# Kernel tuning notes

Hardware: AMD Instinct MI355X
Metric: run time of the kernel (lower is better)

Reference implementation:

```python
import jax, jax.numpy as jnp
import numpy as np

N_NODES = 100000
N_EDGES = 400000
IN_DIM = 69        # torchdrug default atom feature dim
HIDDEN = 256
NUM_CLASSES = 2
NUM_GRAPHS = 4096


def gcn_conv(x, W, b, src, dst, n_nodes):
    """PyG GCNConv: out = D^{-1/2}(A+I)D^{-1/2} (x W) + b (self-loops added)."""
    h = x @ W  # [N, out_dim]
    loop = jnp.arange(n_nodes, dtype=src.dtype)
    s = jnp.concatenate([src, loop])  # sources incl. self loops
    d = jnp.concatenate([dst, loop])  # targets incl. self loops
    deg = jax.ops.segment_sum(jnp.ones_like(d, dtype=h.dtype), d, num_segments=n_nodes)
    dinv = jnp.where(deg > 0, jax.lax.rsqrt(deg), 0.0)
    norm = dinv[s] * dinv[d]  # [E+N]
    msgs = h[s] * norm[:, None]  # gather + scale
    out = jax.ops.segment_sum(msgs, d, num_segments=n_nodes)  # scatter-add
    return out + b


def setup_inputs() -> dict:
    key = jax.random.key(0)
    ks = jax.random.split(key, 16)
    x = jax.random.normal(ks[0], (N_NODES, IN_DIM), dtype=jnp.float32)
    edge_index = jax.random.randint(ks[1], (2, N_EDGES), 0, N_NODES, dtype=jnp.int64)
    batch = jnp.sort(jax.random.randint(ks[2], (N_NODES,), 0, NUM_GRAPHS, dtype=jnp.int64))

    def glorot(k, fan_in, fan_out):
        lim = np.sqrt(6.0 / (fan_in + fan_out)).astype(np.float32)
        return jax.random.uniform(k, (fan_in, fan_out), jnp.float32, -lim, lim)

    W1 = glorot(ks[3], IN_DIM, HIDDEN)
    W2 = glorot(ks[4], HIDDEN, HIDDEN)
    W3 = glorot(ks[5], HIDDEN, HIDDEN)
    W4 = glorot(ks[6], HIDDEN, HIDDEN)
    b1 = jnp.zeros((HIDDEN,), jnp.float32)
    b2 = jnp.zeros((HIDDEN,), jnp.float32)
    b3 = jnp.zeros((HIDDEN,), jnp.float32)
    b4 = jnp.zeros((HIDDEN,), jnp.float32)
    Wl = glorot(ks[7], HIDDEN, NUM_CLASSES)
    bl = jnp.zeros((NUM_CLASSES,), jnp.float32)
    return {"x": x, "edge_index": edge_index, "batch": batch,
            "W1": W1, "b1": b1, "W2": W2, "b2": b2,
            "W3": W3, "b3": b3, "W4": W4, "b4": b4,
            "Wl": Wl, "bl": bl}


def reference(x, edge_index, batch, W1, b1, W2, b2, W3, b3, W4, b4, Wl, bl):
    src, dst = edge_index[0], edge_index[1]
    n = x.shape[0]
    h = jax.nn.relu(gcn_conv(x, W1, b1, src, dst, n))
    h = jax.nn.relu(gcn_conv(h, W2, b2, src, dst, n))
    h = jax.nn.relu(gcn_conv(h, W3, b3, src, dst, n))
    h = gcn_conv(h, W4, b4, src, dst, n)
    # global_mean_pool
    sums = jax.ops.segment_sum(h, batch, num_segments=NUM_GRAPHS)  # [G, H]
    cnts = jax.ops.segment_sum(jnp.ones((n,), h.dtype), batch, num_segments=NUM_GRAPHS)
    pooled = sums / jnp.maximum(cnts, 1.0)[:, None]
    # dropout is identity in eval mode
    return pooled @ Wl + bl  # [G, num_classes]
```

## Files before the change

kernel.cpp:

```cpp
#include <hip/hip_runtime.h>
#include <hip/hip_bf16.h>

#define N_NODES 100000
#define N_EDGES 400000
#define IN_DIM  69
#define KP1     96
#define HID     256
#define NG      4096
#define SCAN_B  391

typedef __attribute__((ext_vector_type(8))) short bf16x8;
typedef __attribute__((ext_vector_type(4))) float f32x4;
typedef unsigned short u16;
typedef unsigned int   u32;

__device__ __forceinline__ float b2f(u16 v) {
    u32 x = ((u32)v) << 16;
    return __builtin_bit_cast(float, x);
}
__device__ __forceinline__ u16 f2b(float f) {
    u32 x = __builtin_bit_cast(u32, f);
    u32 r = (x + 0x7FFF + ((x >> 16) & 1)) >> 16;
    return (u16)r;
}
__device__ __forceinline__ float lo16(u32 v) { return b2f((u16)(v & 0xffff)); }
__device__ __forceinline__ float hi16(u32 v) { return b2f((u16)(v >> 16)); }

__global__ void k_deg(const int* __restrict__ dst, int* __restrict__ deg) {
    int e = blockIdx.x * blockDim.x + threadIdx.x;
    if (e < N_EDGES) atomicAdd(&deg[dst[e]], 1);
}

__global__ void k_dinv(const int* __restrict__ deg, float* __restrict__ dinv) {
    int n = blockIdx.x * blockDim.x + threadIdx.x;
    if (n < N_NODES) dinv[n] = rsqrtf((float)deg[n] + 1.0f);
}

__global__ void k_scan_local(const int* __restrict__ deg, int* __restrict__ rowptr,
                             int* __restrict__ bsum) {
    __shared__ int s[256];
    int tid = threadIdx.x;
    int i = blockIdx.x * 256 + tid;
    int v = (i < N_NODES) ? deg[i] : 0;
    s[tid] = v;
    __syncthreads();
    #pragma unroll
    for (int off = 1; off < 256; off <<= 1) {
        int t = 0;
        if (tid >= off) t = s[tid - off];
        __syncthreads();
        if (tid >= off) s[tid] += t;
        __syncthreads();
    }
    if (i < N_NODES) rowptr[i] = s[tid] - v;
    if (tid == 255) bsum[blockIdx.x] = s[255];
}

__global__ void k_scan_bsum(int* __restrict__ bsum, int* __restrict__ boff) {
    __shared__ int s[512];
    int tid = threadIdx.x;
    int v = (tid < SCAN_B) ? bsum[tid] : 0;
    s[tid] = v;
    __syncthreads();
    #pragma unroll
    for (int off = 1; off < 512; off <<= 1) {
        int t = 0;
        if (tid >= off) t = s[tid - off];
        __syncthreads();
        if (tid >= off) s[tid] += t;
        __syncthreads();
    }
    if (tid < SCAN_B) boff[tid] = s[tid] - v;
}

__global__ void k_scan_add(int* __restrict__ rowptr, const int* __restrict__ boff) {
    int i = blockIdx.x * 256 + threadIdx.x;
    if (i < N_NODES) rowptr[i] += boff[blockIdx.x];
    if (i == 0) rowptr[N_NODES] = N_EDGES;
}

__global__ void k_fill(const int* __restrict__ src, const int* __restrict__ dst,
                       const int* __restrict__ rowptr, int* __restrict__ fill,
                       int* __restrict__ col) {
    int e = blockIdx.x * blockDim.x + threadIdx.x;
    if (e < N_EDGES) {
        int d = dst[e];
        int pos = rowptr[d] + atomicAdd(&fill[d], 1);
        col[pos] = src[e];
    }
}

__global__ void k_gptr(const int* __restrict__ batch, int* __restrict__ gptr) {
    int g = blockIdx.x * 256 + threadIdx.x;
    if (g > NG) return;
    if (g == NG) { gptr[NG] = N_NODES; return; }
    int lo = 0, hi = N_NODES;
    while (lo < hi) {
        int mid = (lo + hi) >> 1;
        if (batch[mid] < g) lo = mid + 1; else hi = mid;
    }
    gptr[g] = lo;
}

__global__ void k_transpose_w(const float* __restrict__ W, u16* __restrict__ Wt, int K, int KP) {
    int k = blockIdx.x;
    int n = threadIdx.x;
    Wt[(size_t)n * KP + k] = (k < K) ? f2b(W[(size_t)k * HID + n]) : (u16)0;
}

__global__ __launch_bounds__(256) void k_pad_scale(const float* __restrict__ x,
                                                   const float* __restrict__ dinv,
                                                   u16* __restrict__ xs) {
    int node = blockIdx.x * 4 + (threadIdx.x >> 6);
    if (node >= N_NODES) return;
    int lane = threadIdx.x & 63;
    if (lane >= 48) return;
    int d0 = lane * 2, d1 = lane * 2 + 1;
    float dv = dinv[node];
    const float* xr = x + (size_t)node * IN_DIM;
    float v0 = (d0 < IN_DIM) ? xr[d0] * dv : 0.0f;
    float v1 = (d1 < IN_DIM) ? xr[d1] * dv : 0.0f;
    u32 o = (u32)f2b(v0) | ((u32)f2b(v1) << 16);
    *(u32*)(xs + (size_t)node * KP1 + d0) = o;
}

__global__ __launch_bounds__(256) void k_agg96(const int* __restrict__ rowptr,
                                               const int* __restrict__ col,
                                               const u16* __restrict__ xs,
                                               const float* __restrict__ dinv,
                                               u16* __restrict__ xa) {
    int node = blockIdx.x * 4 + (threadIdx.x >> 6);
    if (node >= N_NODES) return;
    int lane = threadIdx.x & 63;
    if (lane >= 48) return;
    int j = lane * 2;

    u32 v = *(const u32*)(xs + (size_t)node * KP1 + j);
    float a0 = lo16(v), a1 = hi16(v);
    int e = rowptr[node], end = rowptr[node + 1];
    for (; e + 4 <= end; e += 4) {
        int s0 = col[e], s1 = col[e + 1], s2 = col[e + 2], s3 = col[e + 3];
        u32 w0 = *(const u32*)(xs + (size_t)s0 * KP1 + j);
        u32 w1 = *(const u32*)(xs + (size_t)s1 * KP1 + j);
        u32 w2 = *(const u32*)(xs + (size_t)s2 * KP1 + j);
        u32 w3 = *(const u32*)(xs + (size_t)s3 * KP1 + j);
        a0 += (lo16(w0) + lo16(w1)) + (lo16(w2) + lo16(w3));
        a1 += (hi16(w0) + hi16(w1)) + (hi16(w2) + hi16(w3));
    }
    for (; e < end; ++e) {
        u32 w = *(const u32*)(xs + (size_t)col[e] * KP1 + j);
        a0 += lo16(w); a1 += hi16(w);
    }
    float dv = dinv[node];
    u32 o = (u32)f2b(a0 * dv) | ((u32)f2b(a1 * dv) << 16);
    *(u32*)(xa + (size_t)node * KP1 + j) = o;
}

template<int MODE>
__global__ __launch_bounds__(256) void k_gemm(const u16* __restrict__ A, int KP, int M,
                                              const u16* __restrict__ Wt,
                                              const float* __restrict__ dinv,
                                              const float* __restrict__ bias,
                                              u16* __restrict__ Out) {
    __shared__ __align__(16) u16 As[64 * 40];
    __shared__ __align__(16) u16 Bs[256 * 40];

    const int tid  = threadIdx.x;
    const int wave = tid >> 6;
    const int lane = tid & 63;
    const int quad = lane >> 4;
    const int lm   = lane & 15;
    const int m0   = blockIdx.x * 64;

    f32x4 acc[4][4] = {};

    const int ar = tid >> 2;
    const int ai = (tid & 3) * 8;

    for (int kt = 0; kt < KP; kt += 32) {
        __syncthreads();
        {
            int m = m0 + ar;
            uint4 v = make_uint4(0, 0, 0, 0);
            if (m < M) v = *(const uint4*)(A + (size_t)m * KP + kt + ai);
            *(uint4*)(As + ar * 40 + ai) = v;
        }
        #pragma unroll
        for (int p = 0; p < 4; ++p) {
            int n = p * 64 + (tid >> 2);
            uint4 v = *(const uint4*)(Wt + (size_t)n * KP + kt + ai);
            *(uint4*)(Bs + n * 40 + ai) = v;
        }
        __syncthreads();

        bf16x8 af[4], bfr[4];
        #pragma unroll
        for (int rt = 0; rt < 4; ++rt)
            af[rt] = *(const bf16x8*)(As + (rt * 16 + lm) * 40 + quad * 8);
        #pragma unroll
        for (int ct = 0; ct < 4; ++ct)
            bfr[ct] = *(const bf16x8*)(Bs + (wave * 64 + ct * 16 + lm) * 40 + quad * 8);
        #pragma unroll
        for (int rt = 0; rt < 4; ++rt)
            #pragma unroll
            for (int ct = 0; ct < 4; ++ct)
                acc[rt][ct] = __builtin_amdgcn_mfma_f32_16x16x32_bf16(af[rt], bfr[ct], acc[rt][ct], 0, 0, 0);
    }

    #pragma unroll
    for (int rt = 0; rt < 4; ++rt) {
        #pragma unroll
        for (int reg = 0; reg < 4; ++reg) {
            int m = m0 + rt * 16 + quad * 4 + reg;
            if (m >= M) continue;
            float dv = (MODE == 0) ? dinv[m] : 0.0f;
            #pragma unroll
            for (int ct = 0; ct < 4; ++ct) {
                int n = wave * 64 + ct * 16 + lm;
                float v = acc[rt][ct][reg];
                if (MODE == 0) v *= dv;
                else           v = fmaxf(v + bias[n], 0.0f);
                Out[(size_t)m * HID + n] = f2b(v);
            }
        }
    }
}

__global__ __launch_bounds__(256) void k_agg256(const int* __restrict__ rowptr,
                                                const int* __restrict__ col,
                                                const u16* __restrict__ g,
                                                const float* __restrict__ dinv,
                                                const float* __restrict__ bias,
                                                u16* __restrict__ Xout) {
    int node = blockIdx.x * 4 + (threadIdx.x >> 6);
    if (node >= N_NODES) return;
    int lane = threadIdx.x & 63;
    int j = lane * 4;
    const u16* gj = g + j;

    float a0, a1, a2, a3;
    {
        uint2 v = *(const uint2*)(gj + (size_t)node * HID);
        a0 = lo16(v.x); a1 = hi16(v.x); a2 = lo16(v.y); a3 = hi16(v.y);
    }
    int e = rowptr[node], end = rowptr[node + 1];
    for (; e + 4 <= end; e += 4) {
        int s0 = col[e], s1 = col[e + 1], s2 = col[e + 2], s3 = col[e + 3];
        uint2 w0 = *(const uint2*)(gj + (size_t)s0 * HID);
        uint2 w1 = *(const uint2*)(gj + (size_t)s1 * HID);
        uint2 w2 = *(const uint2*)(gj + (size_t)s2 * HID);
        uint2 w3 = *(const uint2*)(gj + (size_t)s3 * HID);
        a0 += (lo16(w0.x) + lo16(w1.x)) + (lo16(w2.x) + lo16(w3.x));
        a1 += (hi16(w0.x) + hi16(w1.x)) + (hi16(w2.x) + hi16(w3.x));
        a2 += (lo16(w0.y) + lo16(w1.y)) + (lo16(w2.y) + lo16(w3.y));
        a3 += (hi16(w0.y) + hi16(w1.y)) + (hi16(w2.y) + hi16(w3.y));
    }
    for (; e < end; ++e) {
        int s = col[e];
        uint2 w = *(const uint2*)(gj + (size_t)s * HID);
        a0 += lo16(w.x); a1 += hi16(w.x); a2 += lo16(w.y); a3 += hi16(w.y);
    }
    float dv = dinv[node];
    float4 bb = *(const float4*)(bias + j);
    a0 = fmaxf(fmaf(a0, dv, bb.x), 0.0f);
    a1 = fmaxf(fmaf(a1, dv, bb.y), 0.0f);
    a2 = fmaxf(fmaf(a2, dv, bb.z), 0.0f);
    a3 = fmaxf(fmaf(a3, dv, bb.w), 0.0f);
    uint2 o;
    o.x = (u32)f2b(a0) | ((u32)f2b(a1) << 16);
    o.y = (u32)f2b(a2) | ((u32)f2b(a3) << 16);
    *(uint2*)(Xout + (size_t)node * HID + j) = o;
}

__global__ void k_w4l(const float* __restrict__ W4, const float* __restrict__ Wl,
                      const float* __restrict__ b4, const float* __restrict__ bl,
                      float* __restrict__ W4l, float* __restrict__ c4) {
    int k = threadIdx.x;
    float s0 = 0.0f, s1 = 0.0f;
    const float* wr = W4 + (size_t)k * HID;
    for (int j = 0; j < HID; ++j) {
        float w = wr[j];
        s0 += w * Wl[j * 2 + 0];
        s1 += w * Wl[j * 2 + 1];
    }
    W4l[k * 2 + 0] = s0;
    W4l[k * 2 + 1] = s1;
    if (k < 2) {
        float s = bl[k];
        for (int j = 0; j < HID; ++j) s += b4[j] * Wl[j * 2 + k];
        c4[k] = s;
    }
}

__global__ __launch_bounds__(256) void k_gemm2col(const u16* __restrict__ X,
                                                  const float* __restrict__ W4l,
                                                  const float* __restrict__ dinv,
                                                  float* __restrict__ g4) {
    __shared__ float2 sW[HID];
    int tid = threadIdx.x;
    sW[tid] = *(const float2*)(W4l + tid * 2);
    __syncthreads();

    int node = blockIdx.x * 4 + (tid >> 6);
    if (node >= N_NODES) return;
    int lane = tid & 63;
    uint2 v = *(const uint2*)(X + (size_t)node * HID + lane * 4);
    float x0 = lo16(v.x), x1 = hi16(v.x), x2 = lo16(v.y), x3 = hi16(v.y);
    float2 w0 = sW[lane * 4 + 0], w1 = sW[lane * 4 + 1];
    float2 w2 = sW[lane * 4 + 2], w3 = sW[lane * 4 + 3];
    float s0 = x0 * w0.x + x1 * w1.x + x2 * w2.x + x3 * w3.x;
    float s1 = x0 * w0.y + x1 * w1.y + x2 * w2.y + x3 * w3.y;
    #pragma unroll
    for (int off = 32; off >= 1; off >>= 1) {
        s0 += __shfl_down(s0, off);
        s1 += __shfl_down(s1, off);
    }
    if (lane == 0) {
        float dv = dinv[node];
        *(float2*)(g4 + (size_t)node * 2) = make_float2(s0 * dv, s1 * dv);
    }
}

__global__ void k_agg2(const int* __restrict__ rowptr, const int* __restrict__ col,
                       const float* __restrict__ g4, const float* __restrict__ dinv,
                       float* __restrict__ h4) {
    int node = blockIdx.x * blockDim.x + threadIdx.x;
    if (node >= N_NODES) return;
    float2 a = *(const float2*)(g4 + (size_t)node * 2);
    int e = rowptr[node], end = rowptr[node + 1];
    for (; e < end; ++e) {
        float2 w = *(const float2*)(g4 + (size_t)col[e] * 2);
        a.x += w.x; a.y += w.y;
    }
    float dv = dinv[node];
    *(float2*)(h4 + (size_t)node * 2) = make_float2(a.x * dv, a.y * dv);
}

__global__ __launch_bounds__(256) void k_pool2(const float* __restrict__ h4,
                                               const int* __restrict__ gptr,
                                               const float* __restrict__ c4,
                                               float* __restrict__ out) {
    int gph = blockIdx.x * 4 + (threadIdx.x >> 6);
    if (gph >= NG) return;
    int lane = threadIdx.x & 63;
    int b = gptr[gph], e = gptr[gph + 1];
    float s0 = 0.0f, s1 = 0.0f;
    for (int n = b + lane; n < e; n += 64) {
        float2 v = *(const float2*)(h4 + (size_t)n * 2);
        s0 += v.x; s1 += v.y;
    }
    #pragma unroll
    for (int off = 32; off >= 1; off >>= 1) {
        s0 += __shfl_down(s0, off);
        s1 += __shfl_down(s1, off);
    }
    if (lane == 0) {
        float inv = 1.0f / fmaxf((float)(e - b), 1.0f);
        out[gph * 2 + 0] = s0 * inv + c4[0];
        out[gph * 2 + 1] = s1 * inv + c4[1];
    }
}

extern "C" void kernel_launch(void* const* d_in, const int* in_sizes, int n_in,
                              void* d_out, int out_size, void* d_ws, size_t ws_size,
                              hipStream_t stream) {
    const float* x   = (const float*)d_in[0];
    const int* ei    = (const int*)d_in[1];
    const int* src   = ei;
    const int* dst   = ei + N_EDGES;
    const int* batch = (const int*)d_in[2];
    const float* W1 = (const float*)d_in[3];  const float* b1 = (const float*)d_in[4];
    const float* W2 = (const float*)d_in[5];  const float* b2 = (const float*)d_in[6];
    const float* W3 = (const float*)d_in[7];  const float* b3 = (const float*)d_in[8];
    const float* W4 = (const float*)d_in[9];  const float* b4 = (const float*)d_in[10];
    const float* Wl = (const float*)d_in[11]; const float* bl = (const float*)d_in[12];
    float* out = (float*)d_out;

    char* p = (char*)d_ws;
    auto take = [&](size_t bytes) { char* r = p; p += (bytes + 255) & ~(size_t)255; return r; };
    size_t zbytes = (size_t)(N_NODES + N_NODES) * 4;
    int*   deg  = (int*)take(zbytes);
    int*   fill = deg + N_NODES;
    float* dinv = (float*)take((size_t)N_NODES * sizeof(float));
    int* rowptr = (int*)take((size_t)(N_NODES + 1) * sizeof(int));
    int* col    = (int*)take((size_t)N_EDGES * sizeof(int));
    int* bsum   = (int*)take((size_t)SCAN_B * sizeof(int));
    int* boff   = (int*)take((size_t)SCAN_B * sizeof(int));
    int* gptr   = (int*)take((size_t)(NG + 1) * sizeof(int));
    float* W4l  = (float*)take((size_t)HID * 2 * sizeof(float));
    float* c4   = (float*)take(2 * sizeof(float));
    float* g4   = (float*)take((size_t)N_NODES * 2 * sizeof(float));
    float* h4   = (float*)take((size_t)N_NODES * 2 * sizeof(float));
    u16* Wt1 = (u16*)take((size_t)HID * KP1 * 2);
    u16* Wt2 = (u16*)take((size_t)HID * HID * 2);
    u16* Wt3 = (u16*)take((size_t)HID * HID * 2);
    u16* Xs  = (u16*)take((size_t)N_NODES * KP1 * 2);
    u16* Xa  = (u16*)take((size_t)N_NODES * KP1 * 2);
    u16* Gbuf = (u16*)take((size_t)N_NODES * HID * 2);
    u16* Xbuf = (u16*)take((size_t)N_NODES * HID * 2);

    hipMemsetAsync(deg, 0, zbytes, stream);

    k_deg<<<(N_EDGES + 255) / 256, 256, 0, stream>>>(dst, deg);
    k_scan_local<<<SCAN_B, 256, 0, stream>>>(deg, rowptr, bsum);
    k_scan_bsum<<<1, 512, 0, stream>>>(bsum, boff);
    k_scan_add<<<SCAN_B, 256, 0, stream>>>(rowptr, boff);
    k_fill<<<(N_EDGES + 255) / 256, 256, 0, stream>>>(src, dst, rowptr, fill, col);
    k_dinv<<<(N_NODES + 255) / 256, 256, 0, stream>>>(deg, dinv);
    k_gptr<<<(NG + 256) / 256, 256, 0, stream>>>(batch, gptr);

    k_transpose_w<<<KP1, 256, 0, stream>>>(W1, Wt1, IN_DIM, KP1);
    k_transpose_w<<<HID, 256, 0, stream>>>(W2, Wt2, HID, HID);
    k_transpose_w<<<HID, 256, 0, stream>>>(W3, Wt3, HID, HID);
    k_w4l<<<1, 256, 0, stream>>>(W4, Wl, b4, bl, W4l, c4);

    const int gemm_grid = (N_NODES + 63) / 64;
    const int nb4       = (N_NODES + 3) / 4;

    k_pad_scale<<<nb4, 256, 0, stream>>>(x, dinv, Xs);
    k_agg96<<<nb4, 256, 0, stream>>>(rowptr, col, Xs, dinv, Xa);
    k_gemm<1><<<gemm_grid, 256, 0, stream>>>(Xa, KP1, N_NODES, Wt1, dinv, b1, Xbuf);
    k_gemm<0><<<gemm_grid, 256, 0, stream>>>(Xbuf, HID, N_NODES, Wt2, dinv, b2, Gbuf);
    k_agg256<<<nb4, 256, 0, stream>>>(rowptr, col, Gbuf, dinv, b2, Xbuf);
    k_gemm<0><<<gemm_grid, 256, 0, stream>>>(Xbuf, HID, N_NODES, Wt3, dinv, b3, Gbuf);
    k_agg256<<<nb4, 256, 0, stream>>>(rowptr, col, Gbuf, dinv, b3, Xbuf);
    k_gemm2col<<<nb4, 256, 0, stream>>>(Xbuf, W4l, dinv, g4);
    k_agg2<<<(N_NODES + 255) / 256, 256, 0, stream>>>(rowptr, col, g4, dinv, h4);
    k_pool2<<<(NG + 3) / 4, 256, 0, stream>>>(h4, gptr, c4, out);
}
```

Before: 440.1 us.

## Retile GEMM to 128x128 with direct global-to-LDS loads and merge prep kernels

The GEMM moves from 64-row tiles covering all 256 columns to 128x128 tiles on a 2D grid, with a K step of 64. Tiles are loaded with global_load_lds into XOR-swizzled shared memory, which avoids a register round trip and bank conflicts. Row bounds checks are dropped by padding the activation buffers to a multiple of 128 rows, and the first layer's K is padded to 128. The dinv computation is folded into the scan, and the weight transposes, W4·Wl fold and graph-pointer search are merged into one launch to cut launch overhead. The risks are reading uninitialised padded rows, which only produce discarded outputs, and the extra work from padding K for layer 1.

```diff
diff --git a/kernel.cpp b/kernel.cpp
--- a/kernel.cpp
+++ b/kernel.cpp
@@ -2,9 +2,11 @@
 #include <hip/hip_bf16.h>
 
 #define N_NODES 100000
+#define M_PAD   100096
 #define N_EDGES 400000
 #define IN_DIM  69
-#define KP1     96
+#define KPX     96
+#define KPA     128
 #define HID     256
 #define NG      4096
 #define SCAN_B  391
@@ -26,22 +28,24 @@
 __device__ __forceinline__ float lo16(u32 v) { return b2f((u16)(v & 0xffff)); }
 __device__ __forceinline__ float hi16(u32 v) { return b2f((u16)(v >> 16)); }
 
+__device__ __forceinline__ void gl_lds16(const u16* g, u16* l) {
+    __builtin_amdgcn_global_load_lds(
+        (const __attribute__((address_space(1))) void*)g,
+        (__attribute__((address_space(3))) void*)l, 16, 0, 0);
+}
+
 __global__ void k_deg(const int* __restrict__ dst, int* __restrict__ deg) {
     int e = blockIdx.x * blockDim.x + threadIdx.x;
     if (e < N_EDGES) atomicAdd(&deg[dst[e]], 1);
 }
 
-__global__ void k_dinv(const int* __restrict__ deg, float* __restrict__ dinv) {
-    int n = blockIdx.x * blockDim.x + threadIdx.x;
-    if (n < N_NODES) dinv[n] = rsqrtf((float)deg[n] + 1.0f);
-}
-
 __global__ void k_scan_local(const int* __restrict__ deg, int* __restrict__ rowptr,
-                             int* __restrict__ bsum) {
+                             int* __restrict__ bsum, float* __restrict__ dinv) {
     __shared__ int s[256];
     int tid = threadIdx.x;
     int i = blockIdx.x * 256 + tid;
     int v = (i < N_NODES) ? deg[i] : 0;
+    if (i < N_NODES) dinv[i] = rsqrtf((float)v + 1.0f);
     s[tid] = v;
     __syncthreads();
     #pragma unroll
@@ -90,22 +94,48 @@
     }
 }
 
-__global__ void k_gptr(const int* __restrict__ batch, int* __restrict__ gptr) {
-    int g = blockIdx.x * 256 + threadIdx.x;
-    if (g > NG) return;
-    if (g == NG) { gptr[NG] = N_NODES; return; }
-    int lo = 0, hi = N_NODES;
-    while (lo < hi) {
-        int mid = (lo + hi) >> 1;
-        if (batch[mid] < g) lo = mid + 1; else hi = mid;
-    }
-    gptr[g] = lo;
-}
-
-__global__ void k_transpose_w(const float* __restrict__ W, u16* __restrict__ Wt, int K, int KP) {
-    int k = blockIdx.x;
-    int n = threadIdx.x;
-    Wt[(size_t)n * KP + k] = (k < K) ? f2b(W[(size_t)k * HID + n]) : (u16)0;
+__global__ void k_prep(const float* __restrict__ W1, const float* __restrict__ W2,
+                       const float* __restrict__ W3, const float* __restrict__ W4,
+                       const float* __restrict__ Wl, const float* __restrict__ b4,
+                       const float* __restrict__ bl, const int* __restrict__ batch,
+                       u16* __restrict__ Wt1, u16* __restrict__ Wt2, u16* __restrict__ Wt3,
+                       float* __restrict__ W4l, float* __restrict__ c4, int* __restrict__ gptr) {
+    int b = blockIdx.x;
+    int t = threadIdx.x;
+    if (b < KPA) {
+        Wt1[(size_t)t * KPA + b] = (b < IN_DIM) ? f2b(W1[(size_t)b * HID + t]) : (u16)0;
+    } else if (b < KPA + HID) {
+        int k = b - KPA;
+        Wt2[(size_t)t * HID + k] = f2b(W2[(size_t)k * HID + t]);
+    } else if (b < KPA + 2 * HID) {
+        int k = b - KPA - HID;
+        Wt3[(size_t)t * HID + k] = f2b(W3[(size_t)k * HID + t]);
+    } else if (b == KPA + 2 * HID) {
+        float s0 = 0.0f, s1 = 0.0f;
+        const float* wr = W4 + (size_t)t * HID;
+        for (int j = 0; j < HID; ++j) {
+            float w = wr[j];
+            s0 += w * Wl[j * 2 + 0];
+            s1 += w * Wl[j * 2 + 1];
+        }
+        W4l[t * 2 + 0] = s0;
+        W4l[t * 2 + 1] = s1;
+        if (t < 2) {
+            float s = bl[t];
+            for (int j = 0; j < HID; ++j) s += b4[j] * Wl[j * 2 + t];
+            c4[t] = s;
+        }
+    } else {
+        int g = (b - (KPA + 2 * HID + 1)) * 256 + t;
+        if (g > NG) return;
+        if (g == NG) { gptr[NG] = N_NODES; return; }
+        int lo = 0, hi = N_NODES;
+        while (lo < hi) {
+            int mid = (lo + hi) >> 1;
+            if (batch[mid] < g) lo = mid + 1; else hi = mid;
+        }
+        gptr[g] = lo;
+    }
 }
 
 __global__ __launch_bounds__(256) void k_pad_scale(const float* __restrict__ x,
@@ -121,7 +151,7 @@
     float v0 = (d0 < IN_DIM) ? xr[d0] * dv : 0.0f;
     float v1 = (d1 < IN_DIM) ? xr[d1] * dv : 0.0f;
     u32 o = (u32)f2b(v0) | ((u32)f2b(v1) << 16);
-    *(u32*)(xs + (size_t)node * KP1 + d0) = o;
+    *(u32*)(xs + (size_t)node * KPX + d0) = o;
 }
 
 __global__ __launch_bounds__(256) void k_agg96(const int* __restrict__ rowptr,
@@ -132,91 +162,98 @@
     int node = blockIdx.x * 4 + (threadIdx.x >> 6);
     if (node >= N_NODES) return;
     int lane = threadIdx.x & 63;
-    if (lane >= 48) return;
+    if (lane >= 48) {
+        *(u32*)(xa + (size_t)node * KPA + lane * 2) = 0;
+        return;
+    }
     int j = lane * 2;
-
-    u32 v = *(const u32*)(xs + (size_t)node * KP1 + j);
+    u32 v = *(const u32*)(xs + (size_t)node * KPX + j);
     float a0 = lo16(v), a1 = hi16(v);
     int e = rowptr[node], end = rowptr[node + 1];
     for (; e + 4 <= end; e += 4) {
         int s0 = col[e], s1 = col[e + 1], s2 = col[e + 2], s3 = col[e + 3];
-        u32 w0 = *(const u32*)(xs + (size_t)s0 * KP1 + j);
-        u32 w1 = *(const u32*)(xs + (size_t)s1 * KP1 + j);
-        u32 w2 = *(const u32*)(xs + (size_t)s2 * KP1 + j);
-        u32 w3 = *(const u32*)(xs + (size_t)s3 * KP1 + j);
+        u32 w0 = *(const u32*)(xs + (size_t)s0 * KPX + j);
+        u32 w1 = *(const u32*)(xs + (size_t)s1 * KPX + j);
+        u32 w2 = *(const u32*)(xs + (size_t)s2 * KPX + j);
+        u32 w3 = *(const u32*)(xs + (size_t)s3 * KPX + j);
         a0 += (lo16(w0) + lo16(w1)) + (lo16(w2) + lo16(w3));
         a1 += (hi16(w0) + hi16(w1)) + (hi16(w2) + hi16(w3));
     }
     for (; e < end; ++e) {
-        u32 w = *(const u32*)(xs + (size_t)col[e] * KP1 + j);
+        u32 w = *(const u32*)(xs + (size_t)col[e] * KPX + j);
         a0 += lo16(w); a1 += hi16(w);
     }
     float dv = dinv[node];
     u32 o = (u32)f2b(a0 * dv) | ((u32)f2b(a1 * dv) << 16);
-    *(u32*)(xa + (size_t)node * KP1 + j) = o;
+    *(u32*)(xa + (size_t)node * KPA + j) = o;
 }
 
 template<int MODE>
-__global__ __launch_bounds__(256) void k_gemm(const u16* __restrict__ A, int KP, int M,
+__global__ __launch_bounds__(256) void k_gemm(const u16* __restrict__ A, int KP,
                                               const u16* __restrict__ Wt,
                                               const float* __restrict__ dinv,
                                               const float* __restrict__ bias,
                                               u16* __restrict__ Out) {
-    __shared__ __align__(16) u16 As[64 * 40];
-    __shared__ __align__(16) u16 Bs[256 * 40];
+    __shared__ __align__(16) u16 As[128 * 64];
+    __shared__ __align__(16) u16 Bs[128 * 64];
 
     const int tid  = threadIdx.x;
     const int wave = tid >> 6;
     const int lane = tid & 63;
     const int quad = lane >> 4;
     const int lm   = lane & 15;
-    const int m0   = blockIdx.x * 64;
+    const int wr   = wave >> 1;
+    const int wc   = wave & 1;
+    const int m0   = blockIdx.x * 128;
+    const int n0   = blockIdx.y * 128;
 
     f32x4 acc[4][4] = {};
 
-    const int ar = tid >> 2;
-    const int ai = (tid & 3) * 8;
-
-    for (int kt = 0; kt < KP; kt += 32) {
-        __syncthreads();
-        {
-            int m = m0 + ar;
-            uint4 v = make_uint4(0, 0, 0, 0);
-            if (m < M) v = *(const uint4*)(A + (size_t)m * KP + kt + ai);
-            *(uint4*)(As + ar * 40 + ai) = v;
-        }
+    const int sr = lane >> 3;
+    const int sc = lane & 7;
+    const int gc = sc ^ (sr & 7);
+
+    for (int kt = 0; kt < KP; kt += 64) {
+        __syncthreads();
         #pragma unroll
-        for (int p = 0; p < 4; ++p) {
-            int n = p * 64 + (tid >> 2);
-            uint4 v = *(const uint4*)(Wt + (size_t)n * KP + kt + ai);
-            *(uint4*)(Bs + n * 40 + ai) = v;
-        }
-        __syncthreads();
-
-        bf16x8 af[4], bfr[4];
+        for (int i = 0; i < 4; ++i) {
+            int s = wave * 4 + i;
+            int r = s * 8 + sr;
+            const u16* ga = A  + (size_t)(m0 + r) * KP + kt + gc * 8;
+            const u16* gb = Wt + (size_t)(n0 + r) * KP + kt + gc * 8;
+            gl_lds16(ga, As + s * 512);
+            gl_lds16(gb, Bs + s * 512);
+        }
+        __syncthreads();
+
         #pragma unroll
-        for (int rt = 0; rt < 4; ++rt)
-            af[rt] = *(const bf16x8*)(As + (rt * 16 + lm) * 40 + quad * 8);
-        #pragma unroll
-        for (int ct = 0; ct < 4; ++ct)
-            bfr[ct] = *(const bf16x8*)(Bs + (wave * 64 + ct * 16 + lm) * 40 + quad * 8);
-        #pragma unroll
-        for (int rt = 0; rt < 4; ++rt)
+        for (int st = 0; st < 2; ++st) {
+            bf16x8 af[4], bfr[4];
+            const int slot = ((st * 4 + quad) ^ (lm & 7)) * 8;
+            #pragma unroll
+            for (int rt = 0; rt < 4; ++rt)
+                af[rt] = *(const bf16x8*)(As + (wr * 64 + rt * 16 + lm) * 64 + slot);
             #pragma unroll
             for (int ct = 0; ct < 4; ++ct)
-                acc[rt][ct] = __builtin_amdgcn_mfma_f32_16x16x32_bf16(af[rt], bfr[ct], acc[rt][ct], 0, 0, 0);
+                bfr[ct] = *(const bf16x8*)(Bs + (wc * 64 + ct * 16 + lm) * 64 + slot);
+            #pragma unroll
+            for (int rt = 0; rt < 4; ++rt)
+                #pragma unroll
+                for (int ct = 0; ct < 4; ++ct)
+                    acc[rt][ct] = __builtin_amdgcn_mfma_f32_16x16x32_bf16(af[rt], bfr[ct], acc[rt][ct], 0, 0, 0);
+        }
     }
 
     #pragma unroll
     for (int rt = 0; rt < 4; ++rt) {
         #pragma unroll
         for (int reg = 0; reg < 4; ++reg) {
-            int m = m0 + rt * 16 + quad * 4 + reg;
-            if (m >= M) continue;
+            int m = m0 + wr * 64 + rt * 16 + quad * 4 + reg;
+            if (m >= N_NODES) continue;
             float dv = (MODE == 0) ? dinv[m] : 0.0f;
             #pragma unroll
             for (int ct = 0; ct < 4; ++ct) {
-                int n = wave * 64 + ct * 16 + lm;
+                int n = n0 + wc * 64 + ct * 16 + lm;
                 float v = acc[rt][ct][reg];
                 if (MODE == 0) v *= dv;
                 else           v = fmaxf(v + bias[n], 0.0f);
@@ -270,26 +307,6 @@
     o.x = (u32)f2b(a0) | ((u32)f2b(a1) << 16);
     o.y = (u32)f2b(a2) | ((u32)f2b(a3) << 16);
     *(uint2*)(Xout + (size_t)node * HID + j) = o;
-}
-
-__global__ void k_w4l(const float* __restrict__ W4, const float* __restrict__ Wl,
-                      const float* __restrict__ b4, const float* __restrict__ bl,
-                      float* __restrict__ W4l, float* __restrict__ c4) {
-    int k = threadIdx.x;
-    float s0 = 0.0f, s1 = 0.0f;
-    const float* wr = W4 + (size_t)k * HID;
-    for (int j = 0; j < HID; ++j) {
-        float w = wr[j];
-        s0 += w * Wl[j * 2 + 0];
-        s1 += w * Wl[j * 2 + 1];
-    }
-    W4l[k * 2 + 0] = s0;
-    W4l[k * 2 + 1] = s1;
-    if (k < 2) {
-        float s = bl[k];
-        for (int j = 0; j < HID; ++j) s += b4[j] * Wl[j * 2 + k];
-        c4[k] = s;
-    }
 }
 
 __global__ __launch_bounds__(256) void k_gemm2col(const u16* __restrict__ X,
@@ -391,38 +408,33 @@
     float* c4   = (float*)take(2 * sizeof(float));
     float* g4   = (float*)take((size_t)N_NODES * 2 * sizeof(float));
     float* h4   = (float*)take((size_t)N_NODES * 2 * sizeof(float));
-    u16* Wt1 = (u16*)take((size_t)HID * KP1 * 2);
+    u16* Wt1 = (u16*)take((size_t)HID * KPA * 2);
     u16* Wt2 = (u16*)take((size_t)HID * HID * 2);
     u16* Wt3 = (u16*)take((size_t)HID * HID * 2);
-    u16* Xs  = (u16*)take((size_t)N_NODES * KP1 * 2);
-    u16* Xa  = (u16*)take((size_t)N_NODES * KP1 * 2);
+    u16* Xs  = (u16*)take((size_t)N_NODES * KPX * 2);
+    u16* Xa  = (u16*)take((size_t)M_PAD * KPA * 2);
     u16* Gbuf = (u16*)take((size_t)N_NODES * HID * 2);
-    u16* Xbuf = (u16*)take((size_t)N_NODES * HID * 2);
+    u16* Xbuf = (u16*)take((size_t)M_PAD * HID * 2);
 
     hipMemsetAsync(deg, 0, zbytes, stream);
 
     k_deg<<<(N_EDGES + 255) / 256, 256, 0, stream>>>(dst, deg);
-    k_scan_local<<<SCAN_B, 256, 0, stream>>>(deg, rowptr, bsum);
+    k_scan_local<<<SCAN_B, 256, 0, stream>>>(deg, rowptr, bsum, dinv);
     k_scan_bsum<<<1, 512, 0, stream>>>(bsum, boff);
     k_scan_add<<<SCAN_B, 256, 0, stream>>>(rowptr, boff);
     k_fill<<<(N_EDGES + 255) / 256, 256, 0, stream>>>(src, dst, rowptr, fill, col);
-    k_dinv<<<(N_NODES + 255) / 256, 256, 0, stream>>>(deg, dinv);
-    k_gptr<<<(NG + 256) / 256, 256, 0, stream>>>(batch, gptr);
-
-    k_transpose_w<<<KP1, 256, 0, stream>>>(W1, Wt1, IN_DIM, KP1);
-    k_transpose_w<<<HID, 256, 0, stream>>>(W2, Wt2, HID, HID);
-    k_transpose_w<<<HID, 256, 0, stream>>>(W3, Wt3, HID, HID);
-    k_w4l<<<1, 256, 0, stream>>>(W4, Wl, b4, bl, W4l, c4);
-
-    const int gemm_grid = (N_NODES + 63) / 64;
-    const int nb4       = (N_NODES + 3) / 4;
+    k_prep<<<KPA + 2 * HID + 1 + (NG + 256) / 256, 256, 0, stream>>>(
+        W1, W2, W3, W4, Wl, b4, bl, batch, Wt1, Wt2, Wt3, W4l, c4, gptr);
+
+    const int nb4 = (N_NODES + 3) / 4;
+    const dim3 gemm_grid(M_PAD / 128, HID / 128);
 
     k_pad_scale<<<nb4, 256, 0, stream>>>(x, dinv, Xs);
     k_agg96<<<nb4, 256, 0, stream>>>(rowptr, col, Xs, dinv, Xa);
-    k_gemm<1><<<gemm_grid, 256, 0, stream>>>(Xa, KP1, N_NODES, Wt1, dinv, b1, Xbuf);
-    k_gemm<0><<<gemm_grid, 256, 0, stream>>>(Xbuf, HID, N_NODES, Wt2, dinv, b2, Gbuf);
+    k_gemm<1><<<gemm_grid, 256, 0, stream>>>(Xa, KPA, Wt1, dinv, b1, Xbuf);
+    k_gemm<0><<<gemm_grid, 256, 0, stream>>>(Xbuf, HID, Wt2, dinv, b2, Gbuf);
     k_agg256<<<nb4, 256, 0, stream>>>(rowptr, col, Gbuf, dinv, b2, Xbuf);
-    k_gemm<0><<<gemm_grid, 256, 0, stream>>>(Xbuf, HID, N_NODES, Wt3, dinv, b3, Gbuf);
+    k_gemm<0><<<gemm_grid, 256, 0, stream>>>(Xbuf, HID, Wt3, dinv, b3, Gbuf);
     k_agg256<<<nb4, 256, 0, stream>>>(rowptr, col, Gbuf, dinv, b3, Xbuf);
     k_gemm2col<<<nb4, 256, 0, stream>>>(Xbuf, W4l, dinv, g4);
     k_agg2<<<(N_NODES + 255) / 256, 256, 0, stream>>>(rowptr, col, g4, dinv, h4);
```

After: 427.0 us. -3.0%, faster.
